# Optimization experiments

Measured on AMD Instinct MI355X. Metric: run time of the kernel, lower is better.

Reference implementation:

```python
import jax, jax.numpy as jnp
import numpy as np


def setup_inputs() -> dict:
    key = jax.random.key(0)
    k1, k2 = jax.random.split(key)
    x = jax.random.normal(k1, (64, 64, 64, 64), dtype=jnp.float32)
    embeddings = jax.random.normal(k2, (400, 64), dtype=jnp.float32) * 0.1
    return {"x": x, "embeddings": embeddings}


def reference(x, embeddings):
    D = embeddings.shape[1]
    flat_x = x.reshape(-1, D)  # [N, D]
    # squared L2 distance via sum-of-squares + matmul: [N, K]
    distances = (
        jnp.sum(flat_x * flat_x, axis=1, keepdims=True)
        + jnp.sum(embeddings * embeddings, axis=1)
        - 2.0 * jnp.matmul(flat_x, embeddings.T)
    )
    encoding_indices = jnp.argmin(distances, axis=1)  # [N]
    quantized = jnp.take(embeddings, encoding_indices, axis=0)  # [N, D]
    return quantized.reshape(x.shape)
```

## Files before the change

kernel.cpp:

```cpp
#include <hip/hip_runtime.h>

#define D 64
#define K 400
#define KT 25
#define BLOCK 512
#define WPB (BLOCK / 64)

typedef _Float16 f16x8 __attribute__((ext_vector_type(8)));
typedef float f32x4 __attribute__((ext_vector_type(4)));
typedef int i32x4 __attribute__((ext_vector_type(4)));


#define SPL(hh, ll, j, val)                          \
  do {                                               \
    float v_ = (val);                                \
    _Float16 t_ = (_Float16)v_;                      \
    (hh)[j] = t_;                                    \
    (ll)[j] = (_Float16)((v_ - (float)t_) * 2048.0f);\
  } while (0)

__global__ __launch_bounds__(BLOCK, 2) void vq_mfma(
    const float* __restrict__ x,
    const float* __restrict__ emb,
    float* __restrict__ out,
    int nrows) {
  __shared__ __align__(16) _Float16 sB[KT][4][64][8];
  __shared__ float s_norm[K];

  const int tid = threadIdx.x;

  for (int e = tid; e < KT * 4 * 64; e += BLOCK) {
    int t = e >> 8;
    int f = (e >> 6) & 3;
    int l = e & 63;
    int code = t * 16 + (l & 15);
    int kb = ((l >> 4) << 3) + ((f >> 1) << 5);
    const float* ep = emb + code * D + kb;
    float4 u = *(const float4*)ep;
    float4 w = *(const float4*)(ep + 4);
    f16x8 h;
    if ((f & 1) == 0) {
      h[0] = (_Float16)(2.0f * u.x);
      h[1] = (_Float16)(2.0f * u.y);
      h[2] = (_Float16)(2.0f * u.z);
      h[3] = (_Float16)(2.0f * u.w);
      h[4] = (_Float16)(2.0f * w.x);
      h[5] = (_Float16)(2.0f * w.y);
      h[6] = (_Float16)(2.0f * w.z);
      h[7] = (_Float16)(2.0f * w.w);
    } else {
#define LOC(j, val)                                    \
      do {                                             \
        float s_ = 2.0f * (val);                       \
        _Float16 t_ = (_Float16)s_;                    \
        h[j] = (_Float16)((s_ - (float)t_) * 2048.0f); \
      } while (0)
      LOC(0, u.x); LOC(1, u.y); LOC(2, u.z); LOC(3, u.w);
      LOC(4, w.x); LOC(5, w.y); LOC(6, w.z); LOC(7, w.w);
#undef LOC
    }
    *(f16x8*)&sB[t][f][l][0] = h;
  }
  for (int k = tid; k < K; k += BLOCK) {
    const float4* ep = (const float4*)(emb + (size_t)k * D);
    float4 s4 = {0.f, 0.f, 0.f, 0.f};
#pragma unroll
    for (int d = 0; d < 16; ++d) {
      float4 v = ep[d];
      s4.x = fmaf(v.x, v.x, s4.x);
      s4.y = fmaf(v.y, v.y, s4.y);
      s4.z = fmaf(v.z, v.z, s4.z);
      s4.w = fmaf(v.w, v.w, s4.w);
    }
    s_norm[k] = (s4.x + s4.y) + (s4.z + s4.w);
  }
  __syncthreads();

  const int lane = tid & 63;
  const int wid = tid >> 6;
  const int gw = blockIdx.x * WPB + wid;
  const int nw = gridDim.x * WPB;
  const int l15 = lane & 15;
  const int q = lane >> 4;

#define LOADX(a)                                                   \
  do {                                                             \
    const float* xp_ = x + (size_t)(row0 + (a)*16 + l15) * D + q * 8; \
    float4 u0_ = *(const float4*)xp_;                              \
    float4 u1_ = *(const float4*)(xp_ + 4);                        \
    float4 w0_ = *(const float4*)(xp_ + 32);                       \
    float4 w1_ = *(const float4*)(xp_ + 36);                       \
    SPL(xh##a##0, xl##a##0, 0, u0_.x);                             \
    SPL(xh##a##0, xl##a##0, 1, u0_.y);                             \
    SPL(xh##a##0, xl##a##0, 2, u0_.z);                             \
    SPL(xh##a##0, xl##a##0, 3, u0_.w);                             \
    SPL(xh##a##0, xl##a##0, 4, u1_.x);                             \
    SPL(xh##a##0, xl##a##0, 5, u1_.y);                             \
    SPL(xh##a##0, xl##a##0, 6, u1_.z);                             \
    SPL(xh##a##0, xl##a##0, 7, u1_.w);                             \
    SPL(xh##a##1, xl##a##1, 0, w0_.x);                             \
    SPL(xh##a##1, xl##a##1, 1, w0_.y);                             \
    SPL(xh##a##1, xl##a##1, 2, w0_.z);                             \
    SPL(xh##a##1, xl##a##1, 3, w0_.w);                             \
    SPL(xh##a##1, xl##a##1, 4, w1_.x);                             \
    SPL(xh##a##1, xl##a##1, 5, w1_.y);                             \
    SPL(xh##a##1, xl##a##1, 6, w1_.z);                             \
    SPL(xh##a##1, xl##a##1, 7, w1_.w);                             \
  } while (0)

#define PROCA(a)                                                              \
  do {                                                                        \
    f32x4 ah_ = {nn, nn, nn, nn};                                             \
    f32x4 al_ = {0.f, 0.f, 0.f, 0.f};                                         \
    ah_ = __builtin_amdgcn_mfma_f32_16x16x32_f16(xh##a##0, b0, ah_, 0, 0, 0); \
    ah_ = __builtin_amdgcn_mfma_f32_16x16x32_f16(xh##a##1, b2, ah_, 0, 0, 0); \
    al_ = __builtin_amdgcn_mfma_f32_16x16x32_f16(xh##a##0, b1, al_, 0, 0, 0); \
    al_ = __builtin_amdgcn_mfma_f32_16x16x32_f16(xl##a##0, b0, al_, 0, 0, 0); \
    al_ = __builtin_amdgcn_mfma_f32_16x16x32_f16(xh##a##1, b3, al_, 0, 0, 0); \
    al_ = __builtin_amdgcn_mfma_f32_16x16x32_f16(xl##a##1, b2, al_, 0, 0, 0); \
    _Pragma("unroll") for (int i_ = 0; i_ < 4; ++i_) {                        \
      float m_ = fmaf(al_[i_], 4.8828125e-4f, ah_[i_]);    \
      bool gt_ = m_ > bm##a[i_];                                              \
      bm##a[i_] = gt_ ? m_ : bm##a[i_];                                       \
      bt##a[i_] = gt_ ? t : bt##a[i_];                                        \
    }                                                                         \
  } while (0)

#define RSTA(a, mm)                                                        \
  _Pragma("unroll") for (int i_ = 0; i_ < 4; ++i_) {                       \
    float ov_ = __shfl_xor(bm##a[i_], (mm), 64);                           \
    int ok_ = __shfl_xor(bk##a[i_], (mm), 64);                             \
    bool tk_ = (ov_ > bm##a[i_]) || ((ov_ == bm##a[i_]) && (ok_ < bk##a[i_])); \
    bm##a[i_] = tk_ ? ov_ : bm##a[i_];                                     \
    bk##a[i_] = tk_ ? ok_ : bk##a[i_];                                     \
  }

#define WRA(a)                                                \
  do {                                                        \
    int j_ = (lane >> 2) & 3;                                 \
    int k01_ = (j_ & 1) ? bk##a[1] : bk##a[0];                \
    int k23_ = (j_ & 1) ? bk##a[3] : bk##a[2];                \
    int kk_ = (j_ & 2) ? k23_ : k01_;                         \
    int r_ = row0 + (a)*16 + (lane >> 2);                     \
    const f32x4* src_ = (const f32x4*)(emb + (size_t)kk_ * D);\
    f32x4* dst_ = (f32x4*)(out + (size_t)r_ * D);             \
    _Pragma("unroll") for (int s_ = 0; s_ < 4; ++s_) {        \
      int idx_ = (lane & 3) + (s_ << 2);                      \
      dst_[idx_] = src_[idx_];                                \
    }                                                         \
  } while (0)

  const int ngrp = nrows >> 6;
  for (int g = gw; g < ngrp; g += nw) {
    const int row0 = g << 6;

    f16x8 xh00, xh01, xl00, xl01;
    f16x8 xh10, xh11, xl10, xl11;
    f16x8 xh20, xh21, xl20, xl21;
    f16x8 xh30, xh31, xl30, xl31;
    LOADX(0);
    LOADX(1);
    LOADX(2);
    LOADX(3);

    f32x4 bm0, bm1, bm2, bm3;
    i32x4 bt0, bt1, bt2, bt3;
    bm0 = bm1 = bm2 = bm3 = (f32x4){-3.4e38f, -3.4e38f, -3.4e38f, -3.4e38f};
    bt0 = bt1 = bt2 = bt3 = (i32x4){0, 0, 0, 0};

    for (int t = 0; t < KT; ++t) {
      f16x8 b0 = *(const f16x8*)&sB[t][0][lane][0];
      f16x8 b1 = *(const f16x8*)&sB[t][1][lane][0];
      f16x8 b2 = *(const f16x8*)&sB[t][2][lane][0];
      f16x8 b3 = *(const f16x8*)&sB[t][3][lane][0];
      float nn = -s_norm[t * 16 + l15];
      PROCA(0);
      PROCA(1);
      PROCA(2);
      PROCA(3);
    }

    i32x4 bk0 = bt0 * 16 + l15;
    i32x4 bk1 = bt1 * 16 + l15;
    i32x4 bk2 = bt2 * 16 + l15;
    i32x4 bk3 = bt3 * 16 + l15;
#pragma unroll
    for (int mm = 1; mm <= 8; mm <<= 1) {
      RSTA(0, mm)
      RSTA(1, mm)
      RSTA(2, mm)
      RSTA(3, mm)
    }

    WRA(0);
    WRA(1);
    WRA(2);
    WRA(3);
  }
#undef LOADX
#undef PROCA
#undef RSTA
#undef WRA
}

extern "C" void kernel_launch(void* const* d_in, const int* in_sizes, int n_in,
                              void* d_out, int out_size, void* d_ws, size_t ws_size,
                              hipStream_t stream) {
  const float* x = (const float*)d_in[0];
  const float* emb = (const float*)d_in[1];
  float* out = (float*)d_out;
  int nrows = in_sizes[0] / D;
  vq_mfma<<<512, BLOCK, 0, stream>>>(x, emb, out, nrows);
}
```

Before: 162.5 us.

## Precompute split-fp16 codebook in separate kernel and read it from global memory

Moves the per-block codebook conversion (fp16 hi/lo split) and the norm computation into a small prep kernel that writes them to workspace. The main kernel then reads B fragments and norms straight from global memory (L1/L2-cached) instead of LDS. Blocks shrink to 256 threads, the grid doubles, and the occupancy hint is dropped. This removes the redundant per-block prologue and its barrier, but adds a second launch and uses cached global loads in the inner loop instead of LDS reads.

Result: faster. 154.3 us (-5.0%).

```diff
diff --git a/kernel.cpp b/kernel.cpp
--- a/kernel.cpp
+++ b/kernel.cpp
@@ -3,36 +3,23 @@
 #define D 64
 #define K 400
 #define KT 25
-#define BLOCK 512
+#define BLOCK 256
 #define WPB (BLOCK / 64)
+#define NRM_OFF 102400
 
 typedef _Float16 f16x8 __attribute__((ext_vector_type(8)));
 typedef float f32x4 __attribute__((ext_vector_type(4)));
 typedef int i32x4 __attribute__((ext_vector_type(4)));
 
 
-#define SPL(hh, ll, j, val)                          \
-  do {                                               \
-    float v_ = (val);                                \
-    _Float16 t_ = (_Float16)v_;                      \
-    (hh)[j] = t_;                                    \
-    (ll)[j] = (_Float16)((v_ - (float)t_) * 2048.0f);\
-  } while (0)
-
-__global__ __launch_bounds__(BLOCK, 2) void vq_mfma(
-    const float* __restrict__ x,
-    const float* __restrict__ emb,
-    float* __restrict__ out,
-    int nrows) {
-  __shared__ __align__(16) _Float16 sB[KT][4][64][8];
-  __shared__ float s_norm[K];
-
-  const int tid = threadIdx.x;
-
-  for (int e = tid; e < KT * 4 * 64; e += BLOCK) {
-    int t = e >> 8;
-    int f = (e >> 6) & 3;
-    int l = e & 63;
+__global__ void vq_prep(const float* __restrict__ emb, void* __restrict__ ws) {
+  _Float16* B = (_Float16*)ws;
+  float* nrm = (float*)((char*)ws + NRM_OFF);
+  int gid = blockIdx.x * blockDim.x + threadIdx.x;
+  if (gid < KT * 4 * 64) {
+    int t = gid >> 8;
+    int f = (gid >> 6) & 3;
+    int l = gid & 63;
     int code = t * 16 + (l & 15);
     int kb = ((l >> 4) << 3) + ((f >> 1) << 5);
     const float* ep = emb + code * D + kb;
@@ -59,10 +46,10 @@
       LOC(4, w.x); LOC(5, w.y); LOC(6, w.z); LOC(7, w.w);
 #undef LOC
     }
-    *(f16x8*)&sB[t][f][l][0] = h;
-  }
-  for (int k = tid; k < K; k += BLOCK) {
-    const float4* ep = (const float4*)(emb + (size_t)k * D);
+    *(f16x8*)&B[gid * 8] = h;
+  }
+  if (gid < K) {
+    const float4* ep = (const float4*)(emb + (size_t)gid * D);
     float4 s4 = {0.f, 0.f, 0.f, 0.f};
 #pragma unroll
     for (int d = 0; d < 16; ++d) {
@@ -72,10 +59,28 @@
       s4.z = fmaf(v.z, v.z, s4.z);
       s4.w = fmaf(v.w, v.w, s4.w);
     }
-    s_norm[k] = (s4.x + s4.y) + (s4.z + s4.w);
-  }
-  __syncthreads();
-
+    nrm[gid] = (s4.x + s4.y) + (s4.z + s4.w);
+  }
+}
+
+#define SPL(hh, ll, j, val)                          \
+  do {                                               \
+    float v_ = (val);                                \
+    _Float16 t_ = (_Float16)v_;                      \
+    (hh)[j] = t_;                                    \
+    (ll)[j] = (_Float16)((v_ - (float)t_) * 2048.0f);\
+  } while (0)
+
+__global__ __launch_bounds__(BLOCK) void vq_mfma(
+    const float* __restrict__ x,
+    const float* __restrict__ emb,
+    const void* __restrict__ ws,
+    float* __restrict__ out,
+    int nrows) {
+  const f16x8* B = (const f16x8*)ws;
+  const float* nrm = (const float*)((const char*)ws + NRM_OFF);
+
+  const int tid = threadIdx.x;
   const int lane = tid & 63;
   const int wid = tid >> 6;
   const int gw = blockIdx.x * WPB + wid;
@@ -169,11 +174,11 @@
     bt0 = bt1 = bt2 = bt3 = (i32x4){0, 0, 0, 0};
 
     for (int t = 0; t < KT; ++t) {
-      f16x8 b0 = *(const f16x8*)&sB[t][0][lane][0];
-      f16x8 b1 = *(const f16x8*)&sB[t][1][lane][0];
-      f16x8 b2 = *(const f16x8*)&sB[t][2][lane][0];
-      f16x8 b3 = *(const f16x8*)&sB[t][3][lane][0];
-      float nn = -s_norm[t * 16 + l15];
+      f16x8 b0 = B[(t * 4 + 0) * 64 + lane];
+      f16x8 b1 = B[(t * 4 + 1) * 64 + lane];
+      f16x8 b2 = B[(t * 4 + 2) * 64 + lane];
+      f16x8 b3 = B[(t * 4 + 3) * 64 + lane];
+      float nn = -nrm[t * 16 + l15];
       PROCA(0);
       PROCA(1);
       PROCA(2);
@@ -210,5 +215,6 @@
   const float* emb = (const float*)d_in[1];
   float* out = (float*)d_out;
   int nrows = in_sizes[0] / D;
-  vq_mfma<<<512, BLOCK, 0, stream>>>(x, emb, out, nrows);
+  vq_prep<<<25, 256, 0, stream>>>(emb, d_ws);
+  vq_mfma<<<1024, BLOCK, 0, stream>>>(x, emb, d_ws, out, nrows);
 }
```
